# Performance work log

Measured on AMD Instinct MI355X. Metric: run time of the kernel, lower is better.

## Reference

```python
import jax, jax.numpy as jnp
import numpy as np
from jax import lax

V, E, H, B, P, Q = 50000, 300, 256, 32, 400, 40


def _cell(x, h, c, Wih, Whh, b):
    # torch nn.LSTMCell math (b = b_ih + b_hh), gate order i,f,g,o
    g = x @ Wih.T + h @ Whh.T + b
    i, f, gg, o = jnp.split(g, 4, axis=-1)
    c2 = jax.nn.sigmoid(f) * c + jax.nn.sigmoid(i) * jnp.tanh(gg)
    return jax.nn.sigmoid(o) * jnp.tanh(c2), c2


def setup_inputs():
    key = jax.random.key(0)
    ks = jax.random.split(key, 26)
    n = lambda k, s: jax.random.normal(k, s, jnp.float32) * 0.05
    return {
        "passage_ids": jax.random.randint(ks[0], (P, B), 0, V),
        "question_ids": jax.random.randint(ks[1], (Q, B), 0, V),
        "passage_lens": jax.random.randint(ks[2], (B,), P // 2, P + 1),
        "question_lens": jax.random.randint(ks[3], (B,), Q // 2, Q + 1),
        "answer": jax.random.randint(ks[4], (2, B), 0, P // 2),
        "embed": n(ks[5], (V, E)),
        "pre_Wih": n(ks[6], (4 * H, E)),
        "pre_Whh": n(ks[7], (4 * H, H)),
        "pre_b": n(ks[8], (4 * H,)),
        "Wq": n(ks[9], (H, H)),
        "Wp": n(ks[10], (H, H)),
        "bp": n(ks[11], (H,)),
        "Wh": n(ks[12], (H, H)),
        "w_alpha": n(ks[13], (H,)),
        "b_alpha": n(ks[14], ()),
        "m_Wih": n(ks[15], (4 * H, 2 * H)),
        "m_Whh": n(ks[16], (4 * H, H)),
        "m_b": n(ks[17], (4 * H,)),
        "Wm": n(ks[18], (2 * H, H)),
        "Wa": n(ks[19], (H, H)),
        "ba": n(ks[20], (H,)),
        "w_beta": n(ks[21], (H,)),
        "b_beta": n(ks[22], ()),
        "p_Wih": n(ks[23], (4 * H, 2 * H)),
        "p_Whh": n(ks[24], (4 * H, H)),
        "p_b": n(ks[25], (4 * H,)),
    }


def _forward(embed, pre_Wih, pre_Whh, pre_b, Wq, Wp, bp, Wh, w_alpha, b_alpha,
             m_Wih, m_Whh, m_b, Wm, Wa, ba, w_beta, b_beta, p_Wih, p_Whh, p_b,
             passage_ids, passage_lens, question_ids, question_lens):
    Hd = pre_Whh.shape[1]
    Bd = passage_ids.shape[1]
    z0 = jnp.zeros((Bd, Hd), jnp.float32)

    def preprocess(ids, lens):
        x = embed[ids]                                       # [T,B,E]
        T = x.shape[0]
        m = (jnp.arange(T)[:, None] < lens[None, :]).astype(jnp.float32)[:, :, None]  # [T,B,1]
        def step(carry, inp):
            h, c = carry
            xt, mt = inp
            _, c2 = _cell(xt, h, c, pre_Wih, pre_Whh, pre_b)
            h2 = jnp.tanh(c2) * mt                           # module quirk: h := tanh(c)
            return (h2, c2 * mt), h2
        _, Hs = lax.scan(step, (z0, z0), (x, m))
        return Hs, m

    Hp, mP = preprocess(passage_ids, passage_lens)           # [P,B,H]
    Hq, _ = preprocess(question_ids, question_lens)          # [Q,B,H]

    attQ = Hq @ Wq                                           # [Q,B,H]

    def match(Hp_dir, m_dir):
        def step(carry, inp):
            h, c = carry
            hp, mt = inp                                     # hp [B,H], mt [B,1]
            g = jnp.tanh(attQ + hp @ Wp + bp + h @ Wh)       # [Q,B,H]
            alpha = jax.nn.softmax(g @ w_alpha + b_alpha, axis=0)  # softmax over question time [Q,B]
            wq = jnp.einsum('qb,qbh->bh', alpha, Hq)
            zt = jnp.concatenate([hp, wq], axis=-1) * mt
            h2, c2 = _cell(zt, h, c, m_Wih, m_Whh, m_b)
            h2 = h2 * mt
            return (h2, c2 * mt), h2
        _, Hs = lax.scan(step, (z0, z0), (Hp_dir, m_dir))
        return Hs

    Hf = match(Hp, mP)
    Hb = match(Hp[::-1], mP[::-1])[::-1]
    Hr = jnp.concatenate([Hf, Hb], axis=-1)                  # [P,B,2H]

    attM = Hr @ Wm                                           # [P,B,H]
    valid = (jnp.arange(Hr.shape[0])[:, None] < passage_lens[None, :]).astype(jnp.float32)  # [P,B]
    ha, ca = z0, z0
    dists = []
    for _ in range(2):                                       # start / end pointer
        Fk = jnp.tanh(attM + ha @ Wa + ba)                   # [P,B,H]
        scores = Fk @ w_beta + b_beta                        # [P,B]
        scores = jnp.where(valid > 0, scores, -1e30)
        beta = jax.nn.softmax(scores, axis=0) * valid        # zeros past passage length, like original
        dists.append(beta.T)                                 # [B,P]
        wHr = jnp.einsum('pb,pbh->bh', beta, Hr)
        ha, ca = _cell(wHr, ha, ca, p_Wih, p_Whh, p_b)
    return jnp.stack(dists)                                  # [2,B,P]


def reference(passage_ids, question_ids, passage_lens, question_lens, answer,
              embed, pre_Wih, pre_Whh, pre_b, Wq, Wp, bp, Wh, w_alpha, b_alpha,
              m_Wih, m_Whh, m_b, Wm, Wa, ba, w_beta, b_beta, p_Wih, p_Whh, p_b):
    # `answer` only feeds the training loss in the original; forward returns the distributions.
    return _forward(embed, pre_Wih, pre_Whh, pre_b, Wq, Wp, bp, Wh, w_alpha, b_alpha,
                    m_Wih, m_Whh, m_b, Wm, Wa, ba, w_beta, b_beta, p_Wih, p_Whh, p_b,
                    passage_ids, passage_lens, question_ids, question_lens)
```

## Files before the change

kernel.cpp:

```cpp
#include <hip/hip_runtime.h>
#include <hip/hip_bf16.h>

typedef __attribute__((ext_vector_type(8))) short short8;
typedef __attribute__((ext_vector_type(4))) float f32x4;
typedef __attribute__((ext_vector_type(2))) float f32x2;
typedef unsigned short u16;
typedef unsigned int u32;

#define DEV __device__ __forceinline__

static constexpr int Hd    = 256;
static constexpr int Bb    = 32;
static constexpr int Pp    = 400;
static constexpr int Qq    = 40;
static constexpr int NROWS = Pp * Bb + Qq * Bb;
static constexpr int PROBE_MAGIC = 1234567;
static constexpr int NPROBE = 14;

DEV float bf2f(u16 u) { u32 i = ((u32)u) << 16; float f; __builtin_memcpy(&f, &i, 4); return f; }
DEV u16 f2bf(float f) { u32 i; __builtin_memcpy(&i, &f, 4); i += 0x7FFFu + ((i >> 16) & 1u); return (u16)(i >> 16); }
DEV float sigf(float x) { return __builtin_amdgcn_rcpf(1.f + __expf(-x)); }
DEV float tanhf_(float x) {
  float ax = __builtin_fabsf(x);
  float t = __expf(2.f * ax);
  float r = 1.f - 2.f * __builtin_amdgcn_rcpf(t + 1.f);
  return x < 0.f ? -r : r;
}
DEV f32x4 mfma32(short8 a, short8 b, f32x4 c) {
  return __builtin_amdgcn_mfma_f32_16x16x32_bf16(a, b, c, 0, 0, 0);
}
DEV short8 zero8() { short8 z = {0,0,0,0,0,0,0,0}; return z; }

DEV void ast32(u32* p, u32 v) { __hip_atomic_store(p, v, __ATOMIC_RELAXED, __HIP_MEMORY_SCOPE_AGENT); }
DEV u32 pack_pair(u16 mine, int lane) {
  int other = __shfl_xor((int)mine, 1, 64);
  return (lane & 1) ? 0u : ((u32)mine | ((u32)other << 16));
}

struct KArgs {
  const int *pids, *qids, *plen, *qlen;
  const float *embedF, *preWihF, *preWhhF, *preBF, *WqF, *WpF, *bpF, *WhF,
              *walphaF, *balphaF, *mWihF, *mWhhF, *mBF, *WmF, *WaF, *baF,
              *wbetaF, *bbetaF, *pWihF, *pWhhF, *pBF;
  int* bar;
  u16 *WqT, *WpT, *WmT, *WihP, *Xpad, *preX, *Hp, *Hq, *Hrb, *wqR, *wHr, *haB,
      *attQb, *pWihB, *pWhhB, *mWxb, *WhTb, *xW;
  float *hpWp, *attM, *scores, *aWa, *gatesW;
  float* out;
};

DEV void probe_mark(int* bar, int idx) {
  if (blockIdx.x == 0 && threadIdx.x == 0)
    __hip_atomic_store(bar + 768 + idx, PROBE_MAGIC, __ATOMIC_RELEASE, __HIP_MEMORY_SCOPE_AGENT);
}

DEV void barn(int* flagbase, int gi, int gen) {
  __syncthreads();
  if (threadIdx.x == 0)
    __hip_atomic_store((u32*)flagbase + gi, (u32)gen, __ATOMIC_RELEASE, __HIP_MEMORY_SCOPE_AGENT);
  if (threadIdx.x < 16) {
    while (__hip_atomic_load((u32*)flagbase + threadIdx.x, __ATOMIC_RELAXED, __HIP_MEMORY_SCOPE_AGENT) < (u32)gen)
      __builtin_amdgcn_s_sleep(4);
  }
  __syncthreads();
}

__global__ __launch_bounds__(256) void k_prep(KArgs A) {
  const int gtid = blockIdx.x * 256 + threadIdx.x;
  const int GS = 256 * 256;
  for (int idx = gtid; idx < 1024 * 160; idx += GS) {
    int row = idx / 160, cd = idx - row * 160;
    u32 v = 0;
    if (cd < 150) {
      f32x2 e2 = *(const f32x2*)(A.preWihF + (size_t)row * 300 + cd * 2);
      v = (u32)f2bf(e2[0]) | ((u32)f2bf(e2[1]) << 16);
    }
    *(u32*)(A.WihP + (size_t)row * 320 + cd * 2) = v;
  }
  for (int idx = gtid; idx < NROWS * 160; idx += GS) {
    int row = idx / 160, cd = idx - row * 160;
    int id = (row < Pp * Bb) ? A.pids[row] : A.qids[row - Pp * Bb];
    u32 v = 0;
    if (cd < 150) {
      f32x2 e2 = *(const f32x2*)(A.embedF + (size_t)id * 300 + cd * 2);
      v = (u32)f2bf(e2[0]) | ((u32)f2bf(e2[1]) << 16);
    }
    *(u32*)(A.Xpad + (size_t)row * 320 + cd * 2) = v;
  }
  for (int idx = gtid; idx < 65536; idx += GS) {
    int r = idx >> 8, c = idx & 255;
    A.WqT[idx]  = f2bf(A.WqF[c * 256 + r]);
    A.WpT[idx]  = f2bf(A.WpF[c * 256 + r]);
    A.WhTb[idx] = f2bf(A.WhF[c * 256 + r]);
  }
  for (int idx = gtid; idx < 131072; idx += GS) {
    int r = idx >> 9, c = idx & 511;
    A.WmT[idx] = f2bf(A.WmF[c * 256 + r]);
  }
  for (int idx = gtid; idx < 1024 * 256; idx += GS) {
    int n = idx >> 8, k = idx & 255;
    A.mWxb[idx] = f2bf(A.mWihF[(size_t)n * 512 + k]);
  }
  for (int idx = gtid; idx < 524288 + 262144; idx += GS) {
    if (idx < 524288) A.pWihB[idx] = f2bf(A.pWihF[idx]);
    else              A.pWhhB[idx - 524288] = f2bf(A.pWhhF[idx - 524288]);
  }
  if (gtid < 32 * 256) {
    A.aWa[gtid] = A.baF[gtid & 255];
    A.haB[gtid] = 0;
  }
  probe_mark(A.bar, 0);
}

struct GemmArgs { const u16* Ag; int lda; const u16* Bg; int ldb; int Mt64, Nt64, nk; float* Cf; u16* Cb; int ldc; int* bar; int probe; };

__global__ __launch_bounds__(512) void k_gemm(GemmArgs g) {
  const int tid = threadIdx.x, lane = tid & 63;
  const int r16 = lane & 15, kl = (lane >> 4) * 8;
  const int ntile = g.Mt64 * g.Nt64;
  const int stride = gridDim.x * 8;
  for (int tix = blockIdx.x * 8 + (tid >> 6); tix < ntile; tix += stride) {
    int m0 = (tix / g.Nt64) * 64, n0 = (tix % g.Nt64) * 64;
    f32x4 acc[4][4] = {};
    for (int kb = 0; kb < g.nk; ++kb) {
      int k0 = kb * 32 + kl;
      short8 a[4], b[4];
#pragma unroll
      for (int i = 0; i < 4; ++i) {
        a[i] = *(const short8*)(g.Ag + (size_t)(m0 + i * 16 + r16) * g.lda + k0);
        b[i] = *(const short8*)(g.Bg + (size_t)(n0 + i * 16 + r16) * g.ldb + k0);
      }
#pragma unroll
      for (int mi = 0; mi < 4; ++mi)
#pragma unroll
        for (int ni = 0; ni < 4; ++ni) acc[mi][ni] = mfma32(a[mi], b[ni], acc[mi][ni]);
    }
#pragma unroll
    for (int mi = 0; mi < 4; ++mi)
#pragma unroll
      for (int ni = 0; ni < 4; ++ni)
#pragma unroll
        for (int j = 0; j < 4; ++j) {
          int r = m0 + mi * 16 + (lane >> 4) * 4 + j, cc = n0 + ni * 16 + r16;
          if (g.Cf) g.Cf[(size_t)r * g.ldc + cc] = acc[mi][ni][j];
          else      g.Cb[(size_t)r * g.ldc + cc] = f2bf(acc[mi][ni][j]);
        }
  }
  probe_mark(g.bar, g.probe);
}

__global__ __launch_bounds__(512) void k_prescan(KArgs A) {
  __shared__ __align__(16) unsigned char sm[33280];
  float* PRE = (float*)(sm + 24576);
  float* CL  = (float*)(sm + 30720);
  float* PBL = (float*)(sm + 32768);
  const int blk = blockIdx.x;
  const int gi  = blk & 15;
  const int grp = blk >> 4;
  const int steps  = grp ? Qq : Pp;
  const int* lens  = grp ? A.qlen : A.plen;
  u16* Hs          = grp ? A.Hq : A.Hp;
  const int xoff   = grp ? Pp * Bb : 0;
  int* flags = A.bar + grp * 64;

  const int tid = threadIdx.x, lane = tid & 63, wv = tid >> 6;
  const int r16 = lane & 15, kl = (lane >> 4) * 8;
  const int h0 = gi * 16;

  for (int idx = tid; idx < 48 * 256; idx += 512) {
    int row = idx >> 8, k = idx & 255;
    int gate = (row >> 4) * 256 + h0 + (row & 15);
    int byte = row * 512 + ((2 * k) ^ ((row & 7) << 4));
    *(u16*)(sm + byte) = f2bf(A.preWhhF[(size_t)gate * 256 + k]);
  }
  for (int idx = tid; idx < 32 * 16; idx += 512) CL[idx] = 0.f;
  if (tid < 48) PBL[tid] = A.preBF[(tid >> 4) * 256 + h0 + (tid & 15)];
  __syncthreads();

  const int chainC = tid >> 4, hd = tid & 15;
  int gen = 0;
#pragma unroll 1
  for (int t = 0; t < steps; ++t) {
    size_t xr = (size_t)(xoff + t * 32 + chainC) * 1024 + h0 + hd;
    float xp0 = bf2f(A.preX[xr]);
    float xp1 = bf2f(A.preX[xr + 256]);
    float xp2 = bf2f(A.preX[xr + 512]);

    if (wv < 6) {
      int mi = wv & 1, ni = wv >> 1;
      int chain = mi * 16 + r16;
      f32x4 acc = {0.f, 0.f, 0.f, 0.f};
#pragma unroll
      for (int kb = 0; kb < 8; ++kb) {
        int k0 = kb * 32 + kl;
        short8 a = zero8();
        if (t > 0) a = *(const short8*)(Hs + (size_t)((t - 1) * 32 + chain) * 256 + k0);
        int row = ni * 16 + r16;
        short8 b = *(const short8*)(sm + row * 512 + ((2 * k0) ^ ((row & 7) << 4)));
        acc = mfma32(a, b, acc);
      }
      int col = ni * 16 + r16;
#pragma unroll
      for (int j = 0; j < 4; ++j)
        PRE[(mi * 16 + (lane >> 4) * 4 + j) * 48 + col] = acc[j];
    }
    __syncthreads();
    {
      float ip = PRE[chainC * 48 + hd]      + xp0 + PBL[hd];
      float fp = PRE[chainC * 48 + 16 + hd] + xp1 + PBL[16 + hd];
      float gp = PRE[chainC * 48 + 32 + hd] + xp2 + PBL[32 + hd];
      float c2 = sigf(fp) * CL[chainC * 16 + hd] + sigf(ip) * tanhf_(gp);
      float mt = (t < lens[chainC]) ? 1.f : 0.f;
      float h2 = tanhf_(c2) * mt;
      c2 *= mt;
      CL[chainC * 16 + hd] = c2;
      u32 pk = pack_pair(f2bf(h2), lane);
      if (!(lane & 1))
        ast32((u32*)(Hs + (size_t)(t * 32 + chainC) * 256 + h0 + hd), pk);
    }
    barn(flags, gi, ++gen);
  }
  probe_mark(A.bar, 2);
}

__global__ __launch_bounds__(512, 1) void k_match(KArgs A) {
  __shared__ __align__(16) unsigned char sm[81920];
  float* PRE = (float*)(sm + 65536);
  float* CL  = (float*)(sm + 73728);
  float* EL  = (float*)(sm + 75776);
  float* SL  = (float*)(sm + 77824);
  float* AL  = (float*)(sm + 78336);
  float* BPL = (float*)(sm + 78848);
  float* WAL = (float*)(sm + 79872);
  float* MBL = (float*)(sm + 80896);

  const int blk = blockIdx.x;
  const int gi  = blk & 15;
  const int dir = blk >> 4;
  int* flags = A.bar + (2 + dir) * 64;
  const int tid = threadIdx.x, lane = tid & 63, wv = tid >> 6;
  const int r16 = lane & 15, kl = (lane >> 4) * 8;
  const int h0 = gi * 16;

  for (int idx = tid; idx < 64 * 512; idx += 512) {
    int row = idx >> 9, k = idx & 511;
    int gate = (row >> 4) * 256 + h0 + (row & 15);
    float v = (k < 256) ? A.mWihF[(size_t)gate * 512 + 256 + k]
                        : A.mWhhF[(size_t)gate * 256 + (k - 256)];
    int byte = row * 1024 + ((2 * k) ^ ((row & 7) << 4));
    *(u16*)(sm + byte) = f2bf(v);
  }
  for (int idx = tid; idx < 32 * 16; idx += 512) CL[idx] = 0.f;
  if (tid < 256) { BPL[tid] = A.bpF[tid]; WAL[tid] = A.walphaF[tid]; }
  if (tid < 64) MBL[tid] = A.mBF[(tid >> 4) * 256 + h0 + (tid & 15)];
  __syncthreads();

  const float bAl = A.balphaF[0];
  const int cS = wv >> 2, bS = gi * 2 + cS, q4 = wv & 3;
  const int cW = tid >> 8, hW = tid & 255, bW = gi * 2 + cW;
  const int chainC = tid >> 4, hd = tid & 15;
  const int miG = wv >> 2, niG = wv & 3, chainG = miG * 16 + r16, rowG = niG * 16 + r16;

  float aq[10][4], hqv[40];
#pragma unroll
  for (int i = 0; i < 10; ++i)
#pragma unroll
    for (int j = 0; j < 4; ++j)
      aq[i][j] = bf2f(A.attQb[(size_t)((q4 + 4 * i) * 32 + bS) * 256 + lane + 64 * j]);
#pragma unroll
  for (int q = 0; q < 40; ++q)
    hqv[q] = bf2f(A.Hq[(size_t)(q * 32 + bW) * 256 + hW]);

  int gen = 0;
#pragma unroll 1
  for (int t = 0; t < Pp; ++t) {
    int p  = dir ? (Pp - 1 - t) : t;
    int pp = dir ? (p + 1) : (p - 1);

    float hw[4], xw4[4];
#pragma unroll
    for (int j = 0; j < 4; ++j)
      hw[j] = A.hpWp[(size_t)(p * 32 + bS) * 256 + lane + 64 * j];
#pragma unroll
    for (int g = 0; g < 4; ++g)
      xw4[g] = bf2f(A.xW[(size_t)(p * 32 + chainC) * 1024 + g * 256 + h0 + hd]);

    barn(flags, gi, ++gen);

    if (t == 0) {
      EL[tid] = 0.f;
    } else {
      f32x4 acc0 = {0.f,0.f,0.f,0.f}, acc1 = {0.f,0.f,0.f,0.f};
#pragma unroll
      for (int kb = 0; kb < 8; ++kb) {
        int k0 = kb * 32 + kl;
        short8 a = zero8();
        if (r16 < 2)
          a = *(const short8*)(A.Hrb + (size_t)(pp * 32 + gi * 2 + r16) * 512 + dir * 256 + k0);
        short8 bA = *(const short8*)(A.WhTb + (size_t)(wv * 32 + r16) * 256 + k0);
        short8 bB = *(const short8*)(A.WhTb + (size_t)(wv * 32 + 16 + r16) * 256 + k0);
        acc0 = mfma32(a, bA, acc0);
        acc1 = mfma32(a, bB, acc1);
      }
      if ((lane >> 4) == 0) {
        EL[0 * 256 + wv * 32 + r16]      = acc0[0];
        EL[1 * 256 + wv * 32 + r16]      = acc0[1];
        EL[0 * 256 + wv * 32 + 16 + r16] = acc1[0];
        EL[1 * 256 + wv * 32 + 16 + r16] = acc1[1];
      }
    }
    __syncthreads();
    {
#pragma unroll
      for (int i = 0; i < 10; ++i) {
        int q = q4 + 4 * i;
        float s = 0.f;
#pragma unroll
        for (int j = 0; j < 4; ++j) {
          int h = lane + 64 * j;
          s += WAL[h] * tanhf_(aq[i][j] + hw[j] + BPL[h] + EL[cS * 256 + h]);
        }
#pragma unroll
        for (int off = 32; off; off >>= 1) s += __shfl_xor(s, off, 64);
        if (lane == 0) SL[cS * 40 + q] = s;
      }
    }
    __syncthreads();
    if ((wv & 3) == 0) {
      int c = wv >> 2;
      float x = (lane < 40) ? (SL[c * 40 + lane] + bAl) : -3.4e38f;
      float m = x;
#pragma unroll
      for (int off = 32; off; off >>= 1) m = fmaxf(m, __shfl_xor(m, off, 64));
      float e = (lane < 40) ? __expf(x - m) : 0.f;
      float su = e;
#pragma unroll
      for (int off = 32; off; off >>= 1) su += __shfl_xor(su, off, 64);
      if (lane < 40) AL[c * 40 + lane] = e / su;
    }
    __syncthreads();
    {
      float acc = 0.f;
#pragma unroll 8
      for (int q = 0; q < 40; ++q) acc += AL[cW * 40 + q] * hqv[q];
      float mt = (p < A.plen[bW]) ? 1.f : 0.f;
      u32 pk = pack_pair(f2bf(acc * mt), lane);
      if (!(lane & 1))
        ast32((u32*)(A.wqR + (size_t)t * 16384 + (size_t)(dir * 32 + bW) * 256 + hW), pk);
    }
    f32x4 accG = {0.f, 0.f, 0.f, 0.f};
    if (t > 0) {
#pragma unroll
      for (int kb = 8; kb < 16; ++kb) {
        int k0 = kb * 32 + kl;
        short8 a = *(const short8*)(A.Hrb + (size_t)(pp * 32 + chainG) * 512 + dir * 256 + (k0 - 256));
        short8 b = *(const short8*)(sm + rowG * 1024 + ((2 * k0) ^ ((rowG & 7) << 4)));
        accG = mfma32(a, b, accG);
      }
    }
    barn(flags, gi, ++gen);

    {
      const u16* wqS = A.wqR + (size_t)t * 16384 + (size_t)(dir * 32 + chainG) * 256;
#pragma unroll
      for (int kb = 0; kb < 8; ++kb) {
        int k0 = kb * 32 + kl;
        short8 a = *(const short8*)(wqS + k0);
        short8 b = *(const short8*)(sm + rowG * 1024 + ((2 * k0) ^ ((rowG & 7) << 4)));
        accG = mfma32(a, b, accG);
      }
      int col = niG * 16 + r16;
#pragma unroll
      for (int j = 0; j < 4; ++j)
        PRE[(miG * 16 + (lane >> 4) * 4 + j) * 64 + col] = accG[j];
    }
    __syncthreads();
    {
      float ig = PRE[chainC * 64 + hd]      + MBL[hd]      + xw4[0];
      float fg = PRE[chainC * 64 + 16 + hd] + MBL[16 + hd] + xw4[1];
      float gg = PRE[chainC * 64 + 32 + hd] + MBL[32 + hd] + xw4[2];
      float og = PRE[chainC * 64 + 48 + hd] + MBL[48 + hd] + xw4[3];
      float c2 = sigf(fg) * CL[chainC * 16 + hd] + sigf(ig) * tanhf_(gg);
      float h2 = sigf(og) * tanhf_(c2);
      float mt = (p < A.plen[chainC]) ? 1.f : 0.f;
      c2 *= mt; h2 *= mt;
      CL[chainC * 16 + hd] = c2;
      u32 pk = pack_pair(f2bf(h2), lane);
      if (!(lane & 1))
        ast32((u32*)(A.Hrb + (size_t)(p * 32 + chainC) * 512 + dir * 256 + h0 + hd), pk);
    }
  }
  probe_mark(A.bar, 6);
}

__global__ __launch_bounds__(512) void k_scores(KArgs A, int probe) {
  const int blk = blockIdx.x, tid = threadIdx.x, lane = tid & 63, wv = tid >> 6;
  for (int j = wv; j < 50; j += 8) {
    int id = blk * 50 + j;
    int p = id >> 5, b = id & 31;
    float s = 0.f;
#pragma unroll
    for (int jj = 0; jj < 4; ++jj) {
      int h = lane + 64 * jj;
      s += A.wbetaF[h] * tanhf_(A.attM[(size_t)(p * 32 + b) * 256 + h] + A.aWa[b * 256 + h]);
    }
#pragma unroll
    for (int off = 32; off; off >>= 1) s += __shfl_xor(s, off, 64);
    if (lane == 0)
      A.scores[p * 32 + b] = (p < A.plen[b]) ? (s + A.bbetaF[0]) : -1e30f;
  }
  probe_mark(A.bar, probe);
}

__global__ __launch_bounds__(512) void k_soft(KArgs A, int k, int probe) {
  __shared__ __align__(16) unsigned char sm[2048];
  float* BL = (float*)sm;
  float* RED = (float*)(sm + 1664);
  const int b = blockIdx.x, tid = threadIdx.x, lane = tid & 63, wv = tid >> 6;
  float x = (tid < 400) ? A.scores[tid * 32 + b] : -3.4e38f;
  float m = x;
#pragma unroll
  for (int off = 32; off; off >>= 1) m = fmaxf(m, __shfl_xor(m, off, 64));
  if (lane == 0) RED[wv] = m;
  __syncthreads();
  if (tid == 0) {
    float mm = RED[0];
#pragma unroll
    for (int i = 1; i < 8; ++i) mm = fmaxf(mm, RED[i]);
    RED[0] = mm;
  }
  __syncthreads();
  float M = RED[0];
  float e = (tid < 400) ? __expf(x - M) : 0.f;
  float su = e;
#pragma unroll
  for (int off = 32; off; off >>= 1) su += __shfl_xor(su, off, 64);
  if (lane == 0) RED[8 + wv] = su;
  __syncthreads();
  if (tid == 0) {
    float ss = 0.f;
#pragma unroll
    for (int i = 0; i < 8; ++i) ss += RED[8 + i];
    RED[8] = ss;
  }
  __syncthreads();
  float SUM = RED[8];
  if (tid < 400) {
    float beta = (e / SUM) * ((tid < A.plen[b]) ? 1.f : 0.f);
    A.out[(size_t)(k * 32 + b) * 400 + tid] = beta;
    BL[tid] = beta;
  }
  if (k == 0) {
    __syncthreads();
    float acc = 0.f;
#pragma unroll 4
    for (int p = 0; p < 400; ++p) acc += BL[p] * bf2f(A.Hrb[(size_t)(p * 32 + b) * 512 + tid]);
    A.wHr[b * 512 + tid] = f2bf(acc);
  }
  probe_mark(A.bar, probe);
}

__global__ __launch_bounds__(128) void k_pgates(KArgs A) {
  const int blk = blockIdx.x, tid = threadIdx.x, lane = tid & 63, wv = tid >> 6;
  const int r16 = lane & 15, kl = (lane >> 4) * 8;
  const int g0 = blk * 16;
  const int mi = wv, chain = mi * 16 + r16;
  f32x4 acc = {0.f, 0.f, 0.f, 0.f};
#pragma unroll
  for (int kb = 0; kb < 24; ++kb) {
    int k0 = kb * 32 + kl;
    short8 a, b;
    if (kb < 16) {
      a = *(const short8*)(A.wHr + (size_t)chain * 512 + k0);
      b = *(const short8*)(A.pWihB + (size_t)(g0 + r16) * 512 + k0);
    } else {
      a = *(const short8*)(A.haB + (size_t)chain * 256 + (k0 - 512));
      b = *(const short8*)(A.pWhhB + (size_t)(g0 + r16) * 256 + (k0 - 512));
    }
    acc = mfma32(a, b, acc);
  }
#pragma unroll
  for (int j = 0; j < 4; ++j)
    A.gatesW[(size_t)(mi * 16 + (lane >> 4) * 4 + j) * 1024 + g0 + r16] = acc[j];
  probe_mark(A.bar, 10);
}

__global__ __launch_bounds__(256) void k_pcell(KArgs A) {
  __shared__ float HL[256];
  const int b = blockIdx.x, hd = threadIdx.x;
  {
    float ig = A.gatesW[(size_t)b * 1024 + hd]       + A.pBF[hd];
    float gg = A.gatesW[(size_t)b * 1024 + 512 + hd] + A.pBF[512 + hd];
    float og = A.gatesW[(size_t)b * 1024 + 768 + hd] + A.pBF[768 + hd];
    float c2 = sigf(ig) * tanhf_(gg);
    float h2 = sigf(og) * tanhf_(c2);
    HL[hd] = h2;
    A.haB[b * 256 + hd] = f2bf(h2);
  }
  __syncthreads();
  {
    float acc = A.baF[hd];
#pragma unroll 8
    for (int kk = 0; kk < 256; ++kk) acc += HL[kk] * A.WaF[(size_t)kk * 256 + hd];
    A.aWa[b * 256 + hd] = acc;
  }
  probe_mark(A.bar, 11);
}

__global__ __launch_bounds__(64) void k_diag(KArgs A) {
  if (threadIdx.x == 0 && blockIdx.x == 0) {
    int bad = -1;
    for (int i = 0; i < NPROBE; ++i) {
      int v = __hip_atomic_load(A.bar + 768 + i, __ATOMIC_ACQUIRE, __HIP_MEMORY_SCOPE_AGENT);
      if (v != PROBE_MAGIC) { bad = i; break; }
    }
    if (bad >= 0) {
      float s = 128.f * (float)(1 << bad);
      for (int j = 0; j < 8; ++j) A.out[j] = s;
    }
  }
}

extern "C" void kernel_launch(void* const* d_in, const int* in_sizes, int n_in,
                              void* d_out, int out_size, void* d_ws, size_t ws_size,
                              hipStream_t stream) {
  (void)in_sizes; (void)n_in; (void)ws_size;
  KArgs A;
  A.pids = (const int*)d_in[0];
  A.qids = (const int*)d_in[1];
  A.plen = (const int*)d_in[2];
  A.qlen = (const int*)d_in[3];
  A.embedF  = (const float*)d_in[5];
  A.preWihF = (const float*)d_in[6];
  A.preWhhF = (const float*)d_in[7];
  A.preBF   = (const float*)d_in[8];
  A.WqF     = (const float*)d_in[9];
  A.WpF     = (const float*)d_in[10];
  A.bpF     = (const float*)d_in[11];
  A.WhF     = (const float*)d_in[12];
  A.walphaF = (const float*)d_in[13];
  A.balphaF = (const float*)d_in[14];
  A.mWihF   = (const float*)d_in[15];
  A.mWhhF   = (const float*)d_in[16];
  A.mBF     = (const float*)d_in[17];
  A.WmF     = (const float*)d_in[18];
  A.WaF     = (const float*)d_in[19];
  A.baF     = (const float*)d_in[20];
  A.wbetaF  = (const float*)d_in[21];
  A.bbetaF  = (const float*)d_in[22];
  A.pWihF   = (const float*)d_in[23];
  A.pWhhF   = (const float*)d_in[24];
  A.pBF     = (const float*)d_in[25];

  char* w = (char*)d_ws;
  size_t off = 0;
  auto take = [&](size_t bytes) { void* p = w + off; off += (bytes + 255) & ~(size_t)255; return p; };
  A.bar    = (int*)take(4096);
  A.WqT    = (u16*)take(256 * 256 * 2);
  A.WpT    = (u16*)take(256 * 256 * 2);
  A.WmT    = (u16*)take(256 * 512 * 2);
  A.WihP   = (u16*)take((size_t)1024 * 320 * 2);
  A.Xpad   = (u16*)take((size_t)NROWS * 320 * 2);
  A.preX   = (u16*)take((size_t)NROWS * 1024 * 2);
  A.Hp     = (u16*)take((size_t)Pp * Bb * 256 * 2);
  A.Hq     = (u16*)take((size_t)Qq * Bb * 256 * 2);
  A.Hrb    = (u16*)take((size_t)Pp * Bb * 512 * 2);
  A.wqR    = (u16*)take((size_t)Pp * 2 * 32 * 256 * 2);
  A.wHr    = (u16*)take(32 * 512 * 2);
  A.haB    = (u16*)take(32 * 256 * 2);
  A.attQb  = (u16*)take((size_t)Qq * Bb * 256 * 2);
  A.pWihB  = (u16*)take((size_t)1024 * 512 * 2);
  A.pWhhB  = (u16*)take((size_t)1024 * 256 * 2);
  A.mWxb   = (u16*)take((size_t)1024 * 256 * 2);
  A.WhTb   = (u16*)take((size_t)256 * 256 * 2);
  A.hpWp   = (float*)take((size_t)Pp * Bb * 256 * 4);
  A.attM   = (float*)take((size_t)Pp * Bb * 256 * 4);
  A.scores = (float*)take((size_t)Pp * Bb * 4);
  A.aWa    = (float*)take(32 * 256 * 4);
  A.gatesW = (float*)take((size_t)32 * 1024 * 4);
  A.xW     = A.preX;
  A.out    = (float*)d_out;

  hipMemsetAsync(d_out, 0x3C, 64, stream);
  hipMemsetAsync(A.bar, 0, 4096, stream);

  (void)hipGetLastError();
  size_t outB = (size_t)out_size * 4;
  int li = 0;
#define CK  if (hipGetLastError() != hipSuccess) { hipMemsetAsync(d_out, 0x41 + li, outB, stream); return; } ++li;

  hipLaunchKernelGGL(k_prep, dim3(256), dim3(256), 0, stream, A); CK;

  GemmArgs g1{A.Xpad, 320, A.WihP, 320, NROWS / 64, 16, 10, nullptr, A.preX, 1024, A.bar, 1};
  hipLaunchKernelGGL(k_gemm, dim3(256), dim3(512), 0, stream, g1); CK;

  hipLaunchKernelGGL(k_prescan, dim3(32), dim3(512), 0, stream, A); CK;

  GemmArgs g2{A.Hq, 256, A.WqT, 256, 20, 4, 8, nullptr, A.attQb, 256, A.bar, 3};
  hipLaunchKernelGGL(k_gemm, dim3(16), dim3(512), 0, stream, g2); CK;
  GemmArgs g3{A.Hp, 256, A.WpT, 256, 200, 4, 8, A.hpWp, nullptr, 256, A.bar, 4};
  hipLaunchKernelGGL(k_gemm, dim3(128), dim3(512), 0, stream, g3); CK;
  GemmArgs gx{A.Hp, 256, A.mWxb, 256, 200, 16, 8, nullptr, A.xW, 1024, A.bar, 5};
  hipLaunchKernelGGL(k_gemm, dim3(256), dim3(512), 0, stream, gx); CK;

  hipLaunchKernelGGL(k_match, dim3(32), dim3(512), 0, stream, A); CK;

  GemmArgs g4{A.Hrb, 512, A.WmT, 512, 200, 4, 16, A.attM, nullptr, 256, A.bar, 7};
  hipLaunchKernelGGL(k_gemm, dim3(128), dim3(512), 0, stream, g4); CK;

  hipLaunchKernelGGL(k_scores, dim3(256), dim3(512), 0, stream, A, 8); CK;
  hipLaunchKernelGGL(k_soft,   dim3(32),  dim3(512), 0, stream, A, 0, 9); CK;
  hipLaunchKernelGGL(k_pgates, dim3(64),  dim3(128), 0, stream, A); CK;
  hipLaunchKernelGGL(k_pcell,  dim3(32),  dim3(256), 0, stream, A); CK;
  hipLaunchKernelGGL(k_scores, dim3(256), dim3(512), 0, stream, A, 12); CK;
  hipLaunchKernelGGL(k_soft,   dim3(32),  dim3(512), 0, stream, A, 1, 13); CK;

  hipLaunchKernelGGL(k_diag,   dim3(1),   dim3(64),  0, stream, A); CK;
#undef CK
}
```

Before: 9.127 ms.

## Repartition preprocess LSTM scan by batch chains to drop cross-block barriers

The preprocess LSTM scan now gives each block 4 whole batch chains across all hidden units, instead of splitting the hidden dimension across 16 blocks. The per-step grid-wide flag barrier becomes a plain __syncthreads, and h is kept in LDS. The recurrent weights are pre-packed into MFMA tile order and streamed from global/L2 every step, and only 4 of 16 MFMA rows carry useful data. Elsewhere, bf16 stores are packed into 64-bit quad stores, the barrier flag store is relaxed, and the spin sleep is shorter. The trade is less synchronisation latency against more weight traffic per block and wasted MFMA work.

```diff
diff --git a/kernel.cpp b/kernel.cpp
--- a/kernel.cpp
+++ b/kernel.cpp
@@ -6,6 +6,7 @@
 typedef __attribute__((ext_vector_type(2))) float f32x2;
 typedef unsigned short u16;
 typedef unsigned int u32;
+typedef unsigned long long u64;
 
 #define DEV __device__ __forceinline__
 
@@ -30,11 +31,19 @@
   return __builtin_amdgcn_mfma_f32_16x16x32_bf16(a, b, c, 0, 0, 0);
 }
 DEV short8 zero8() { short8 z = {0,0,0,0,0,0,0,0}; return z; }
-
-DEV void ast32(u32* p, u32 v) { __hip_atomic_store(p, v, __ATOMIC_RELAXED, __HIP_MEMORY_SCOPE_AGENT); }
-DEV u32 pack_pair(u16 mine, int lane) {
-  int other = __shfl_xor((int)mine, 1, 64);
-  return (lane & 1) ? 0u : ((u32)mine | ((u32)other << 16));
+DEV short8 ldtile(const u16* base, int tile, int lane) {
+  return *(const short8*)(base + ((size_t)tile * 64 + lane) * 8);
+}
+
+DEV void ast64(u64* p, u64 v) { __hip_atomic_store(p, v, __ATOMIC_RELAXED, __HIP_MEMORY_SCOPE_AGENT); }
+DEV void quad_store(u16* base_even, u16 mine, int lane) {
+  u32 p01 = (u32)mine | ((u32)(u16)__shfl_xor((int)mine, 1, 64) << 16);
+  u32 p23 = (u32)__shfl_xor((int)p01, 2, 64);
+  if (!(lane & 3)) ast64((u64*)base_even, (u64)p01 | ((u64)p23 << 32));
+}
+DEV void pair_store(u16* base_even, u32 mine2, int lane) {
+  u32 other = (u32)__shfl_xor((int)mine2, 1, 64);
+  if (!(lane & 1)) ast64((u64*)base_even, (u64)mine2 | ((u64)other << 32));
 }
 
 struct KArgs {
@@ -44,7 +53,7 @@
               *wbetaF, *bbetaF, *pWihF, *pWhhF, *pBF;
   int* bar;
   u16 *WqT, *WpT, *WmT, *WihP, *Xpad, *preX, *Hp, *Hq, *Hrb, *wqR, *wHr, *haB,
-      *attQb, *pWihB, *pWhhB, *mWxb, *WhTb, *xW;
+      *attQb, *pWihB, *pWhhB, *mWxb, *WhTb, *preWhT, *xW;
   float *hpWp, *attM, *scores, *aWa, *gatesW;
   float* out;
 };
@@ -57,10 +66,10 @@
 DEV void barn(int* flagbase, int gi, int gen) {
   __syncthreads();
   if (threadIdx.x == 0)
-    __hip_atomic_store((u32*)flagbase + gi, (u32)gen, __ATOMIC_RELEASE, __HIP_MEMORY_SCOPE_AGENT);
+    __hip_atomic_store((u32*)flagbase + gi, (u32)gen, __ATOMIC_RELAXED, __HIP_MEMORY_SCOPE_AGENT);
   if (threadIdx.x < 16) {
     while (__hip_atomic_load((u32*)flagbase + threadIdx.x, __ATOMIC_RELAXED, __HIP_MEMORY_SCOPE_AGENT) < (u32)gen)
-      __builtin_amdgcn_s_sleep(4);
+      __builtin_amdgcn_s_sleep(2);
   }
   __syncthreads();
 }
@@ -100,6 +109,12 @@
   for (int idx = gtid; idx < 1024 * 256; idx += GS) {
     int n = idx >> 8, k = idx & 255;
     A.mWxb[idx] = f2bf(A.mWihF[(size_t)n * 512 + k]);
+  }
+  for (int idx = gtid; idx < 48 * 8 * 512; idx += GS) {
+    int e = idx & 7, l = (idx >> 3) & 63, tk = idx >> 9;
+    int nt = tk >> 3, kt = tk & 7;
+    int n = nt * 16 + (l & 15), k = kt * 32 + (l >> 4) * 8 + e;
+    A.preWhT[idx] = f2bf(A.preWhhF[(size_t)n * 256 + k]);
   }
   for (int idx = gtid; idx < 524288 + 262144; idx += GS) {
     if (idx < 524288) A.pWihB[idx] = f2bf(A.pWihF[idx]);
@@ -149,76 +164,78 @@
   probe_mark(g.bar, g.probe);
 }
 
-__global__ __launch_bounds__(512) void k_prescan(KArgs A) {
-  __shared__ __align__(16) unsigned char sm[33280];
-  float* PRE = (float*)(sm + 24576);
-  float* CL  = (float*)(sm + 30720);
-  float* PBL = (float*)(sm + 32768);
+__global__ __launch_bounds__(512, 1) void k_prescan(KArgs A) {
+  __shared__ __align__(16) unsigned char sm[24576];
+  u16*   HF  = (u16*)sm;
+  float* CS  = (float*)(sm + 2176);
+  float* PRE = (float*)(sm + 6784);
+  float* PBL = (float*)(sm + 19648);
   const int blk = blockIdx.x;
-  const int gi  = blk & 15;
-  const int grp = blk >> 4;
-  const int steps  = grp ? Qq : Pp;
-  const int* lens  = grp ? A.qlen : A.plen;
-  u16* Hs          = grp ? A.Hq : A.Hp;
-  const int xoff   = grp ? Pp * Bb : 0;
-  int* flags = A.bar + grp * 64;
-
+  const int isQ = blk >> 3;
+  const int c0  = (blk & 7) * 4;
+  const int steps = isQ ? Qq : Pp;
+  const int* lens = isQ ? A.qlen : A.plen;
+  u16* Hs = isQ ? A.Hq : A.Hp;
+  const int xoff = isQ ? Pp * Bb : 0;
   const int tid = threadIdx.x, lane = tid & 63, wv = tid >> 6;
   const int r16 = lane & 15, kl = (lane >> 4) * 8;
-  const int h0 = gi * 16;
-
-  for (int idx = tid; idx < 48 * 256; idx += 512) {
-    int row = idx >> 8, k = idx & 255;
-    int gate = (row >> 4) * 256 + h0 + (row & 15);
-    int byte = row * 512 + ((2 * k) ^ ((row & 7) << 4));
-    *(u16*)(sm + byte) = f2bf(A.preWhhF[(size_t)gate * 256 + k]);
-  }
-  for (int idx = tid; idx < 32 * 16; idx += 512) CL[idx] = 0.f;
-  if (tid < 48) PBL[tid] = A.preBF[(tid >> 4) * 256 + h0 + (tid & 15)];
-  __syncthreads();
-
-  const int chainC = tid >> 4, hd = tid & 15;
-  int gen = 0;
+
+  for (int idx = tid; idx < 768; idx += 512) PBL[idx] = A.preBF[idx];
+  for (int idx = tid; idx < 4 * 264; idx += 512) HF[idx] = 0;
+  for (int idx = tid; idx < 4 * 256; idx += 512) CS[idx] = 0.f;
+  __syncthreads();
+
+  const int cC = tid >> 7, hh = (tid & 127) * 2;
+  const int bC = c0 + cC;
+  const int lenC = lens[bC];
+
 #pragma unroll 1
   for (int t = 0; t < steps; ++t) {
-    size_t xr = (size_t)(xoff + t * 32 + chainC) * 1024 + h0 + hd;
-    float xp0 = bf2f(A.preX[xr]);
-    float xp1 = bf2f(A.preX[xr + 256]);
-    float xp2 = bf2f(A.preX[xr + 512]);
-
-    if (wv < 6) {
-      int mi = wv & 1, ni = wv >> 1;
-      int chain = mi * 16 + r16;
+    short8 afr[8];
+#pragma unroll
+    for (int kt = 0; kt < 8; ++kt)
+      afr[kt] = (r16 < 4) ? *(const short8*)(HF + r16 * 264 + kt * 32 + kl) : zero8();
+#pragma unroll
+    for (int i = 0; i < 6; ++i) {
+      int nt = wv * 6 + i;
+      short8 bf[8];
+#pragma unroll
+      for (int kt = 0; kt < 8; ++kt) bf[kt] = ldtile(A.preWhT, nt * 8 + kt, lane);
       f32x4 acc = {0.f, 0.f, 0.f, 0.f};
 #pragma unroll
-      for (int kb = 0; kb < 8; ++kb) {
-        int k0 = kb * 32 + kl;
-        short8 a = zero8();
-        if (t > 0) a = *(const short8*)(Hs + (size_t)((t - 1) * 32 + chain) * 256 + k0);
-        int row = ni * 16 + r16;
-        short8 b = *(const short8*)(sm + row * 512 + ((2 * k0) ^ ((row & 7) << 4)));
-        acc = mfma32(a, b, acc);
-      }
-      int col = ni * 16 + r16;
-#pragma unroll
-      for (int j = 0; j < 4; ++j)
-        PRE[(mi * 16 + (lane >> 4) * 4 + j) * 48 + col] = acc[j];
+      for (int kt = 0; kt < 8; ++kt) acc = mfma32(afr[kt], bf[kt], acc);
+      if ((lane >> 4) == 0) {
+#pragma unroll
+        for (int j = 0; j < 4; ++j) PRE[j * 776 + nt * 16 + r16] = acc[j];
+      }
     }
     __syncthreads();
     {
-      float ip = PRE[chainC * 48 + hd]      + xp0 + PBL[hd];
-      float fp = PRE[chainC * 48 + 16 + hd] + xp1 + PBL[16 + hd];
-      float gp = PRE[chainC * 48 + 32 + hd] + xp2 + PBL[32 + hd];
-      float c2 = sigf(fp) * CL[chainC * 16 + hd] + sigf(ip) * tanhf_(gp);
-      float mt = (t < lens[chainC]) ? 1.f : 0.f;
-      float h2 = tanhf_(c2) * mt;
-      c2 *= mt;
-      CL[chainC * 16 + hd] = c2;
-      u32 pk = pack_pair(f2bf(h2), lane);
-      if (!(lane & 1))
-        ast32((u32*)(Hs + (size_t)(t * 32 + chainC) * 256 + h0 + hd), pk);
-    }
-    barn(flags, gi, ++gen);
+      size_t xr = (size_t)(xoff + t * 32 + bC) * 1024;
+      u32 x0 = *(const u32*)(A.preX + xr + hh);
+      u32 x1 = *(const u32*)(A.preX + xr + 256 + hh);
+      u32 x2 = *(const u32*)(A.preX + xr + 512 + hh);
+      u16 hb[2];
+#pragma unroll
+      for (int u = 0; u < 2; ++u) {
+        int h = hh + u;
+        float xi = bf2f(u ? (u16)(x0 >> 16) : (u16)x0);
+        float xf = bf2f(u ? (u16)(x1 >> 16) : (u16)x1);
+        float xg = bf2f(u ? (u16)(x2 >> 16) : (u16)x2);
+        float ip = PRE[cC * 776 + h]       + xi + PBL[h];
+        float fp = PRE[cC * 776 + 256 + h] + xf + PBL[256 + h];
+        float gp = PRE[cC * 776 + 512 + h] + xg + PBL[512 + h];
+        float c2 = sigf(fp) * CS[cC * 256 + h] + sigf(ip) * tanhf_(gp);
+        float mt = (t < lenC) ? 1.f : 0.f;
+        float h2 = tanhf_(c2) * mt;
+        CS[cC * 256 + h] = c2 * mt;
+        hb[u] = f2bf(h2);
+      }
+      u32 pk = (u32)hb[0] | ((u32)hb[1] << 16);
+      *(u32*)(HF + cC * 264 + hh) = pk;
+      *(u32*)(Hs + (size_t)(t * 32 + bC) * 256 + hh) = pk;
+    }
+    __syncthreads();
   }
   probe_mark(A.bar, 2);
 }
@@ -344,9 +361,8 @@
 #pragma unroll 8
       for (int q = 0; q < 40; ++q) acc += AL[cW * 40 + q] * hqv[q];
       float mt = (p < A.plen[bW]) ? 1.f : 0.f;
-      u32 pk = pack_pair(f2bf(acc * mt), lane);
-      if (!(lane & 1))
-        ast32((u32*)(A.wqR + (size_t)t * 16384 + (size_t)(dir * 32 + bW) * 256 + hW), pk);
+      u16 wb = f2bf(acc * mt);
+      quad_store(A.wqR + (size_t)t * 16384 + (size_t)(dir * 32 + bW) * 256 + (hW & ~3), wb, lane);
     }
     f32x4 accG = {0.f, 0.f, 0.f, 0.f};
     if (t > 0) {
@@ -385,9 +401,8 @@
       float mt = (p < A.plen[chainC]) ? 1.f : 0.f;
       c2 *= mt; h2 *= mt;
       CL[chainC * 16 + hd] = c2;
-      u32 pk = pack_pair(f2bf(h2), lane);
-      if (!(lane & 1))
-        ast32((u32*)(A.Hrb + (size_t)(p * 32 + chainC) * 512 + dir * 256 + h0 + hd), pk);
+      u16 hb = f2bf(h2);
+      quad_store(A.Hrb + (size_t)(p * 32 + chainC) * 512 + dir * 256 + h0 + (hd & ~3), hb, lane);
     }
   }
   probe_mark(A.bar, 6);
@@ -555,31 +570,32 @@
   char* w = (char*)d_ws;
   size_t off = 0;
   auto take = [&](size_t bytes) { void* p = w + off; off += (bytes + 255) & ~(size_t)255; return p; };
-  A.bar    = (int*)take(4096);
-  A.WqT    = (u16*)take(256 * 256 * 2);
-  A.WpT    = (u16*)take(256 * 256 * 2);
-  A.WmT    = (u16*)take(256 * 512 * 2);
-  A.WihP   = (u16*)take((size_t)1024 * 320 * 2);
-  A.Xpad   = (u16*)take((size_t)NROWS * 320 * 2);
-  A.preX   = (u16*)take((size_t)NROWS * 1024 * 2);
-  A.Hp     = (u16*)take((size_t)Pp * Bb * 256 * 2);
-  A.Hq     = (u16*)take((size_t)Qq * Bb * 256 * 2);
-  A.Hrb    = (u16*)take((size_t)Pp * Bb * 512 * 2);
-  A.wqR    = (u16*)take((size_t)Pp * 2 * 32 * 256 * 2);
-  A.wHr    = (u16*)take(32 * 512 * 2);
-  A.haB    = (u16*)take(32 * 256 * 2);
-  A.attQb  = (u16*)take((size_t)Qq * Bb * 256 * 2);
-  A.pWihB  = (u16*)take((size_t)1024 * 512 * 2);
-  A.pWhhB  = (u16*)take((size_t)1024 * 256 * 2);
-  A.mWxb   = (u16*)take((size_t)1024 * 256 * 2);
-  A.WhTb   = (u16*)take((size_t)256 * 256 * 2);
-  A.hpWp   = (float*)take((size_t)Pp * Bb * 256 * 4);
-  A.attM   = (float*)take((size_t)Pp * Bb * 256 * 4);
-  A.scores = (float*)take((size_t)Pp * Bb * 4);
-  A.aWa    = (float*)take(32 * 256 * 4);
-  A.gatesW = (float*)take((size_t)32 * 1024 * 4);
-  A.xW     = A.preX;
-  A.out    = (float*)d_out;
+  A.bar     = (int*)take(4096);
+  A.WqT     = (u16*)take(256 * 256 * 2);
+  A.WpT     = (u16*)take(256 * 256 * 2);
+  A.WmT     = (u16*)take(256 * 512 * 2);
+  A.WihP    = (u16*)take((size_t)1024 * 320 * 2);
+  A.Xpad    = (u16*)take((size_t)NROWS * 320 * 2);
+  A.preX    = (u16*)take((size_t)NROWS * 1024 * 2);
+  A.Hp      = (u16*)take((size_t)Pp * Bb * 256 * 2);
+  A.Hq      = (u16*)take((size_t)Qq * Bb * 256 * 2);
+  A.Hrb     = (u16*)take((size_t)Pp * Bb * 512 * 2);
+  A.wqR     = (u16*)take((size_t)Pp * 2 * 32 * 256 * 2);
+  A.wHr     = (u16*)take(32 * 512 * 2);
+  A.haB     = (u16*)take(32 * 256 * 2);
+  A.attQb   = (u16*)take((size_t)Qq * Bb * 256 * 2);
+  A.pWihB   = (u16*)take((size_t)1024 * 512 * 2);
+  A.pWhhB   = (u16*)take((size_t)1024 * 256 * 2);
+  A.mWxb    = (u16*)take((size_t)1024 * 256 * 2);
+  A.WhTb    = (u16*)take((size_t)256 * 256 * 2);
+  A.preWhT  = (u16*)take((size_t)48 * 8 * 512 * 2);
+  A.hpWp    = (float*)take((size_t)Pp * Bb * 256 * 4);
+  A.attM    = (float*)take((size_t)Pp * Bb * 256 * 4);
+  A.scores  = (float*)take((size_t)Pp * Bb * 4);
+  A.aWa     = (float*)take(32 * 256 * 4);
+  A.gatesW  = (float*)take((size_t)32 * 1024 * 4);
+  A.xW      = A.preX;
+  A.out     = (float*)d_out;
 
   hipMemsetAsync(d_out, 0x3C, 64, stream);
   hipMemsetAsync(A.bar, 0, 4096, stream);
@@ -594,7 +610,7 @@
   GemmArgs g1{A.Xpad, 320, A.WihP, 320, NROWS / 64, 16, 10, nullptr, A.preX, 1024, A.bar, 1};
   hipLaunchKernelGGL(k_gemm, dim3(256), dim3(512), 0, stream, g1); CK;
 
-  hipLaunchKernelGGL(k_prescan, dim3(32), dim3(512), 0, stream, A); CK;
+  hipLaunchKernelGGL(k_prescan, dim3(16), dim3(512), 0, stream, A); CK;
 
   GemmArgs g2{A.Hq, 256, A.WqT, 256, 20, 4, 8, nullptr, A.attQb, 256, A.bar, 3};
   hipLaunchKernelGGL(k_gemm, dim3(16), dim3(512), 0, stream, g2); CK;
```

Result: slower. 9.387 ms (+2.9%).
